# Kernel tuning notes

Measured on AMD Instinct MI355X. Metric: run time of the kernel, lower is better.

The kernel has to match this reference:

```python
import jax, jax.numpy as jnp
import numpy as np

NB, NWAY, NBASE, FEAT, SEM = 8, 16, 8000, 512, 300
TEMP = float(np.sqrt(FEAT))  # d_k = feat_dim // n_head = 512


def setup_inputs() -> dict:
    key = jax.random.key(0)
    ks = jax.random.split(key, 18)
    n = jax.random.normal
    s_q = float(np.sqrt(2.0 / (FEAT + FEAT)))   # std for w_qs/w_ks/w_vs (d_model + d_k)
    s_sem = float(np.sqrt(2.0 / 600.0))
    s_lin = float(np.sqrt(1.0 / 300.0))
    return {
        "support_feat": n(ks[0], (NB, NWAY, FEAT), jnp.float32),
        "base_weights": n(ks[1], (NB, NBASE, FEAT), jnp.float32),
        "support_seman": n(ks[2], (NB, NWAY, SEM), jnp.float32),
        "base_seman": n(ks[3], (NB, NBASE, SEM), jnp.float32),
        # map_sem: Linear(300,300) -> LeakyReLU(0.1) -> Linear(300,300); weights stored (in,out)
        "map_w1": n(ks[4], (SEM, SEM), jnp.float32) * s_lin,
        "map_b1": jnp.zeros((SEM,), jnp.float32),
        "map_w2": n(ks[5], (SEM, SEM), jnp.float32) * s_lin,
        "map_b2": jnp.zeros((SEM,), jnp.float32),
        # task fusion gates: Linear(feat+300 -> feat) and Linear(feat+300 -> 300)
        "visfuse_w": n(ks[6], (FEAT + SEM, FEAT), jnp.float32) * s_lin,
        "visfuse_b": jnp.zeros((FEAT,), jnp.float32),
        "semfuse_w": n(ks[7], (FEAT + SEM, SEM), jnp.float32) * s_lin,
        "semfuse_b": jnp.zeros((SEM,), jnp.float32),
        # MHA projections (bias-free), stored (in,out)
        "w_qs": n(ks[8], (FEAT, FEAT), jnp.float32) * s_q,
        "w_ks": n(ks[9], (FEAT, FEAT), jnp.float32) * s_q,
        "w_vs": n(ks[10], (FEAT, FEAT), jnp.float32) * s_q,
        "w_qs_sem": n(ks[11], (SEM, FEAT), jnp.float32) * s_sem,
        "w_ks_sem": n(ks[12], (SEM, FEAT), jnp.float32) * s_sem,
        "fc_w": n(ks[13], (FEAT, FEAT), jnp.float32) * s_q,
    }


def _map_sem(x, w1, b1, w2, b2):
    return jax.nn.leaky_relu(x @ w1 + b1, negative_slope=0.1) @ w2 + b2


def _forward(support_feat, base_weights, support_seman, base_seman,
             map_w1, map_b1, map_w2, map_b2,
             visfuse_w, visfuse_b, semfuse_w, semfuse_b,
             w_qs, w_ks, w_vs, w_qs_sem, w_ks_sem, fc_w):
    # semantic calibration of both support and base semantics (base_seman_calib=True)
    support_seman = _map_sem(support_seman, map_w1, b1=map_b1, w2=map_w2, b2=map_b2)  # (nb,nway,300)
    base_seman = _map_sem(base_seman, map_w1, b1=map_b1, w2=map_w2, b2=map_b2)        # (nb,N,300)

    # avg_task_mem over base classes (repeat over nway is a no-op for the mean)
    avg = jnp.concatenate([jnp.mean(base_weights, axis=1, keepdims=True),
                           jnp.mean(base_seman, axis=1, keepdims=True)], axis=-1)      # (nb,1,feat+300)
    gate_vis = jax.nn.sigmoid(avg @ visfuse_w + visfuse_b) + 1.0                       # (nb,1,feat)
    gate_sem = jax.nn.sigmoid(avg @ semfuse_w + semfuse_b) + 1.0                       # (nb,1,300)

    base_mem_vis = base_weights                 # un-gated value memory (v)
    k_vis = base_weights * gate_vis             # gated keys
    k_sem = base_seman * gate_sem               # gated semantic keys

    # projections (n_head=1, d_k=d_v=feat)
    q = support_feat @ w_qs                     # (nb,nway,feat)
    k = k_vis @ w_ks                            # (nb,N,feat)
    v = base_mem_vis @ w_vs                     # (nb,N,feat)
    q_tot = q + support_seman @ w_qs_sem        # semantic-fused q
    k_tot = k + k_sem @ w_ks_sem                # semantic-fused k

    # each support sample attends over the shared base memory of its episode
    attn_score = jnp.einsum('bwd,bnd->bwn', q_tot, k_tot) / TEMP                       # (nb,nway,N)
    attn = jax.nn.softmax(attn_score, axis=-1)
    out = jnp.einsum('bwn,bnd->bwd', attn, v) @ fc_w + support_feat                    # residual
    # SupportCalibrator returns (support_center, support_attn=attn_score)
    return out, attn_score


def reference(support_feat, base_weights, support_seman, base_seman,
              map_w1, map_b1, map_w2, map_b2,
              visfuse_w, visfuse_b, semfuse_w, semfuse_b,
              w_qs, w_ks, w_vs, w_qs_sem, w_ks_sem, fc_w):
    return _forward(support_feat, base_weights, support_seman, base_seman,
                    map_w1, map_b1, map_w2, map_b2,
                    visfuse_w, visfuse_b, semfuse_w, semfuse_b,
                    w_qs, w_ks, w_vs, w_qs_sem, w_ks_sem, fc_w)
```

## Files before the change

kernel.cpp:

```cpp
#include <hip/hip_runtime.h>

#define NB 8
#define NWAY 16
#define NBASE 8000
#define FEAT 512
#define SEM 300
#define CAT (FEAT + SEM)
#define HLD 304

typedef __attribute__((ext_vector_type(8))) short bf16x8;
typedef __attribute__((ext_vector_type(4))) float f32x4;
typedef __attribute__((ext_vector_type(8))) unsigned short us8;
typedef __attribute__((ext_vector_type(4))) unsigned short us4;
typedef __attribute__((ext_vector_type(2))) unsigned short us2;
typedef unsigned short us;

__device__ __forceinline__ us f2bf(float x) {
    union { float f; unsigned int u; } v; v.f = x;
    unsigned int r = v.u + 0x7FFFu + ((v.u >> 16) & 1u);
    return (us)(r >> 16);
}
__device__ __forceinline__ float bf2f(us u) {
    union { unsigned int u; float f; } v; v.u = ((unsigned int)u) << 16;
    return v.f;
}

constexpr long O_BWH   = 0L;
constexpr long O_H     = 65536000L;
constexpr long O_W1T   = 104448000L;
constexpr long O_W2T   = 104652800L;
constexpr long O_QWT   = 104857600L;
constexpr long O_WVST  = 106496000L;
constexpr long O_FCWT  = 107020288L;
constexpr long O_PQT   = 107544576L;
constexpr long O_PMAX  = 107759616L;
constexpr long O_PSUM  = 107791872L;
constexpr long O_RMAX  = 107824128L;
constexpr long O_RINV  = 107824640L;
constexpr long O_F     = 107825152L;
constexpr long O_MBW   = O_F;
constexpr long O_MH    = O_F + 16384;
constexpr long O_GV    = O_F + 25984;
constexpr long O_GS    = O_F + 42368;
constexpr long O_SSMH  = O_F + 77952;
constexpr long O_QTG   = O_F + 77952;
constexpr long O_OV    = O_F + 233600;
constexpr long O_SFH   = O_F + 540800;
constexpr long O_PSG   = O_F + 540800;
constexpr long O_H1G   = O_F + 671872;
constexpr long O_CC    = O_F + 802944;
constexpr long O_WKST  = O_F + 803456;
constexpr long O_WKSST = O_F + 1327744;
constexpr long O_W2N   = O_F + 1655424;
constexpr long O_SSCG  = O_F + 1860224;

__global__ void k_prep(const float* __restrict__ w1, const float* __restrict__ w2,
                       const float* __restrict__ wqs, const float* __restrict__ wqss,
                       const float* __restrict__ wvs, const float* __restrict__ fcw,
                       const float* __restrict__ wks, const float* __restrict__ wkss,
                       const float* __restrict__ sf, const float* __restrict__ ssm,
                       us* __restrict__ w1t, us* __restrict__ w2t, us* __restrict__ qwT,
                       us* __restrict__ wvsT, us* __restrict__ fcwT,
                       us* __restrict__ wksT, us* __restrict__ wkssT, us* __restrict__ w2n,
                       us* __restrict__ sfh, us* __restrict__ ssmh,
                       float* __restrict__ mz, float* __restrict__ cz, us* __restrict__ pqt) {
    long e = (long)blockIdx.x * 256 + threadIdx.x;
    switch (blockIdx.y) {
    case 0: if (e < 320 * 320) { int n = e / 320, k = e % 320;
            w1t[e] = f2bf((n < SEM && k < SEM) ? w1[(long)k * SEM + n] : 0.f); } break;
    case 1: if (e < 320 * 320) { int n = e / 320, k = e % 320;
            w2t[e] = f2bf((n < SEM && k < SEM) ? w2[(long)k * SEM + n] : 0.f); } break;
    case 2: if (e < 512 * 832) { int n = e / 832, k = e % 832;
            float v = 0.f;
            if (k < FEAT) v = wqs[(long)k * FEAT + n];
            else if (k < CAT) v = wqss[(long)(k - FEAT) * FEAT + n];
            qwT[e] = f2bf(v); } break;
    case 3: if (e < 512 * 512) { int n = e / 512, k = e % 512;
            wvsT[e] = f2bf(wvs[(long)k * FEAT + n]); } break;
    case 4: if (e < 512 * 512) { int n = e / 512, k = e % 512;
            fcwT[e] = f2bf(fcw[(long)k * FEAT + n]); } break;
    case 5:
        if (e < NB * FEAT + NB * SEM) mz[e] = 0.f;
        if (e < NB * NWAY) cz[e] = 0.f;
        if (e < 128 * 28) pqt[(e / 28) * 840 + 812 + (e % 28)] = 0;
        break;
    case 6: if (e < 512 * 512) wksT[e] = f2bf(wks[e]); break;
    case 7: if (e < 320 * 512) { int n = e / 512, k = e % 512;
            wkssT[e] = (n < SEM) ? f2bf(wkss[(long)n * FEAT + k]) : (us)0; } break;
    case 8: if (e < 320 * 320) { int n = e / 320, k = e % 320;
            w2n[e] = (n < SEM && k < SEM) ? f2bf(w2[(long)n * SEM + k]) : (us)0; } break;
    case 9: if (e < 128 * 512) sfh[e] = f2bf(sf[e]); break;
    case 10: if (e < 128 * 320) { int n = e / 320, k = e % 320;
            ssmh[e] = (k < SEM) ? f2bf(ssm[(long)n * SEM + k]) : (us)0; } break;
    }
}

__global__ __launch_bounds__(256) void k_cvt_mlp1(
        const float* __restrict__ bw, us* __restrict__ bwh, float* __restrict__ mbw,
        const us* __restrict__ ssmh, const us* __restrict__ w1t,
        const float* __restrict__ b1, us* __restrict__ h1g) {
    __shared__ float red[128][4];
    const int bid = blockIdx.x;
    const int t = threadIdx.x;
    if (bid < 10) {
        const int ctile = bid % 5, rh = bid / 5;
        const int wv = t >> 6, lane = t & 63;
        const int m16 = lane & 15, q = lane >> 4;
        const int nc0 = ctile * 64;
        const int n = nc0 + wv * 16 + m16;
        f32x4 acc[4];
        #pragma unroll
        for (int i = 0; i < 4; ++i) acc[i] = (f32x4){0.f, 0.f, 0.f, 0.f};
        for (int ks = 0; ks < 10; ++ks) {
            const int k = ks * 32 + q * 8;
            bf16x8 bb = *(const bf16x8*)(w1t + (long)n * 320 + k);
            #pragma unroll
            for (int mt = 0; mt < 4; ++mt) {
                bf16x8 a = *(const bf16x8*)(ssmh + (long)(rh * 64 + mt * 16 + m16) * 320 + k);
                acc[mt] = __builtin_amdgcn_mfma_f32_16x16x32_bf16(a, bb, acc[mt], 0, 0, 0);
            }
        }
        const int col = n;
        const float bias = (col < SEM) ? b1[col] : 0.f;
        #pragma unroll
        for (int mt = 0; mt < 4; ++mt)
            #pragma unroll
            for (int r = 0; r < 4; ++r) {
                float v = acc[mt][r] + bias;
                v = v > 0.f ? v : 0.1f * v;
                const int gr = rh * 64 + mt * 16 + q * 4 + r;
                h1g[(long)gr * 320 + col] = (col < SEM) ? f2bf(v) : (us)0;
            }
        return;
    }
    const int fb = bid - 10;
    const int b = fb / 125, ch = fb % 125;
    int cg = t & 127, rs = t >> 7;
    long base = ((long)b * NBASE + (long)ch * 64) * FEAT + cg * 4;
    float s0 = 0.f, s1 = 0.f, s2 = 0.f, s3 = 0.f;
    for (int r0 = rs * 4; r0 < 64; r0 += 8) {
        float4 v[4];
        #pragma unroll
        for (int u = 0; u < 4; ++u)
            v[u] = *(const float4*)(bw + base + (long)(r0 + u) * FEAT);
        #pragma unroll
        for (int u = 0; u < 4; ++u) {
            us4 o; o.x = f2bf(v[u].x); o.y = f2bf(v[u].y); o.z = f2bf(v[u].z); o.w = f2bf(v[u].w);
            *(us4*)(bwh + base + (long)(r0 + u) * FEAT) = o;
            s0 += v[u].x; s1 += v[u].y; s2 += v[u].z; s3 += v[u].w;
        }
    }
    if (rs == 1) { red[cg][0] = s0; red[cg][1] = s1; red[cg][2] = s2; red[cg][3] = s3; }
    __syncthreads();
    if (rs == 0) {
        atomicAdd(&mbw[b * FEAT + cg * 4 + 0], s0 + red[cg][0]);
        atomicAdd(&mbw[b * FEAT + cg * 4 + 1], s1 + red[cg][1]);
        atomicAdd(&mbw[b * FEAT + cg * 4 + 2], s2 + red[cg][2]);
        atomicAdd(&mbw[b * FEAT + cg * 4 + 3], s3 + red[cg][3]);
    }
}

__global__ __launch_bounds__(256, 2) void k_hg_mlp2(const float* __restrict__ X,
        const us* __restrict__ W1T, const float* __restrict__ b1,
        us* __restrict__ H, float* __restrict__ mh,
        const us* __restrict__ h1g, const us* __restrict__ w2t,
        const float* __restrict__ b2, us* __restrict__ sscg) {
    __shared__ char smem[128 * 304 * 2];
    const int bid = blockIdx.x;
    const int t = threadIdx.x;
    const int wv = t >> 6, lane = t & 63;
    const int m16 = lane & 15, q = lane >> 4;
    if (bid < 10) {
        const int ctile = bid % 5, rh = bid / 5;
        const int n = ctile * 64 + wv * 16 + m16;
        f32x4 acc[4];
        #pragma unroll
        for (int i = 0; i < 4; ++i) acc[i] = (f32x4){0.f, 0.f, 0.f, 0.f};
        for (int ks = 0; ks < 10; ++ks) {
            const int k = ks * 32 + q * 8;
            bf16x8 bb = *(const bf16x8*)(w2t + (long)n * 320 + k);
            #pragma unroll
            for (int mt = 0; mt < 4; ++mt) {
                bf16x8 a = *(const bf16x8*)(h1g + (long)(rh * 64 + mt * 16 + m16) * 320 + k);
                acc[mt] = __builtin_amdgcn_mfma_f32_16x16x32_bf16(a, bb, acc[mt], 0, 0, 0);
            }
        }
        const int col = n;
        const float bias = (col < SEM) ? b2[col] : 0.f;
        #pragma unroll
        for (int mt = 0; mt < 4; ++mt)
            #pragma unroll
            for (int r = 0; r < 4; ++r) {
                const int gr = rh * 64 + mt * 16 + q * 4 + r;
                sscg[(long)gr * 320 + col] = (col < SEM) ? f2bf(acc[mt][r] + bias) : (us)0;
            }
        return;
    }
    us (*As)[72] = (us(*)[72])smem;
    us (*Bs)[72] = (us(*)[72])(smem + 18432);
    us (*Cs)[HLD] = (us(*)[HLD])smem;
    const int fb = bid - 10;
    const int b = fb / 63;
    const int bm = (fb % 63) * 128;
    const long rowbase = (long)b * NBASE;
    f32x4 acc[8][5];
    #pragma unroll
    for (int i = 0; i < 8; ++i)
        #pragma unroll
        for (int j = 0; j < 5; ++j) acc[i][j] = (f32x4){0.f, 0.f, 0.f, 0.f};
    for (int ks = 0; ks < 5; ++ks) {
        const int k0 = ks * 64;
        #pragma unroll
        for (int it = 0; it < 8; ++it) {
            int c = t + it * 256;
            int row = c >> 4, j = c & 15;
            int gk = k0 + j * 4;
            float4 v = make_float4(0.f, 0.f, 0.f, 0.f);
            if (gk < SEM && bm + row < NBASE)
                v = *(const float4*)(X + (rowbase + bm + row) * SEM + gk);
            us4 u; u.x = f2bf(v.x); u.y = f2bf(v.y); u.z = f2bf(v.z); u.w = f2bf(v.w);
            *(us4*)(&As[row][j * 4]) = u;
        }
        #pragma unroll
        for (int it = 0; it < 10; ++it) {
            int c = t + it * 256;
            int n = c >> 3, j = c & 7;
            int4 v = *(const int4*)(W1T + (long)n * 320 + k0 + j * 8);
            *(int4*)(&Bs[n][j * 8]) = v;
        }
        __syncthreads();
        #pragma unroll
        for (int kc = 0; kc < 64; kc += 32) {
            bf16x8 a[8], bb[5];
            #pragma unroll
            for (int rt = 0; rt < 8; ++rt)
                a[rt] = *(const bf16x8*)(&As[rt * 16 + m16][kc + q * 8]);
            #pragma unroll
            for (int ct = 0; ct < 5; ++ct)
                bb[ct] = *(const bf16x8*)(&Bs[(wv * 5 + ct) * 16 + m16][kc + q * 8]);
            #pragma unroll
            for (int rt = 0; rt < 8; ++rt)
                #pragma unroll
                for (int ct = 0; ct < 5; ++ct)
                    acc[rt][ct] = __builtin_amdgcn_mfma_f32_16x16x32_bf16(a[rt], bb[ct], acc[rt][ct], 0, 0, 0);
        }
        __syncthreads();
    }
    float csum[5] = {0.f, 0.f, 0.f, 0.f, 0.f};
    #pragma unroll
    for (int ct = 0; ct < 5; ++ct) {
        int col = (wv * 5 + ct) * 16 + m16;
        float bias = (col < SEM) ? b1[col] : 0.f;
        #pragma unroll
        for (int rt = 0; rt < 8; ++rt) {
            int rl = rt * 16 + q * 4;
            #pragma unroll
            for (int r = 0; r < 4; ++r) {
                float v = acc[rt][ct][r] + bias;
                v = v > 0.f ? v : 0.1f * v;
                if (col < SEM && bm + rl + r < NBASE) {
                    Cs[rl + r][col] = f2bf(v);
                    csum[ct] += v;
                }
            }
        }
    }
    if (t < 128) *(us4*)(&Cs[t][300]) = (us4){0, 0, 0, 0};
    #pragma unroll
    for (int ct = 0; ct < 5; ++ct) {
        float s = csum[ct];
        s += __shfl_xor(s, 16);
        s += __shfl_xor(s, 32);
        int col = (wv * 5 + ct) * 16 + m16;
        if (q == 0 && col < SEM) atomicAdd(&mh[b * SEM + col], s);
    }
    __syncthreads();
    for (int i = t; i < 128 * 76; i += 256) {
        int row = i / 76, j = i % 76;
        if (bm + row < NBASE)
            *(us4*)(H + (rowbase + bm + row) * HLD + j * 4) = *(const us4*)(&Cs[row][j * 4]);
    }
}

__global__ __launch_bounds__(256) void k_gates_qtot(
        const float* __restrict__ mbw, const float* __restrict__ mh,
        const float* __restrict__ mw2, const float* __restrict__ mb2,
        const float* __restrict__ vfw, const float* __restrict__ vfb,
        const float* __restrict__ sfw, const float* __restrict__ sfb,
        float* __restrict__ gv, float* __restrict__ gs,
        const us* __restrict__ sfh, const us* __restrict__ sscg,
        const us* __restrict__ qwT, us* __restrict__ qtotg) {
    __shared__ float avgL[CAT];
    __shared__ float mhL[SEM];
    __shared__ float red[4][64];
    const int bid = blockIdx.x;
    const int t = threadIdx.x;
    if (bid < 16) {
        const int ctile = bid % 8, rh = bid / 8;
        const int wv = t >> 6, lane = t & 63;
        const int m16 = lane & 15, q = lane >> 4;
        const int n = ctile * 64 + wv * 16 + m16;
        f32x4 acc[4];
        #pragma unroll
        for (int i = 0; i < 4; ++i) acc[i] = (f32x4){0.f, 0.f, 0.f, 0.f};
        for (int ks = 0; ks < 26; ++ks) {
            const int k = ks * 32 + q * 8;
            bf16x8 bb = *(const bf16x8*)(qwT + (long)n * 832 + k);
            #pragma unroll
            for (int mt = 0; mt < 4; ++mt) {
                const int gr = rh * 64 + mt * 16 + m16;
                bf16x8 a = (k < FEAT)
                    ? *(const bf16x8*)(sfh + (long)gr * 512 + k)
                    : *(const bf16x8*)(sscg + (long)gr * 320 + (k - FEAT));
                acc[mt] = __builtin_amdgcn_mfma_f32_16x16x32_bf16(a, bb, acc[mt], 0, 0, 0);
            }
        }
        #pragma unroll
        for (int mt = 0; mt < 4; ++mt)
            #pragma unroll
            for (int r = 0; r < 4; ++r) {
                const int gr = rh * 64 + mt * 16 + q * 4 + r;
                qtotg[(long)gr * 512 + n] = f2bf(acc[mt][r]);
            }
        return;
    }
    const int tile = (bid - 16) % 13, b = (bid - 16) / 13;
    const float invN = 1.0f / NBASE;
    for (int i = t; i < SEM; i += 256) mhL[i] = mh[b * SEM + i] * invN;
    for (int i = t; i < FEAT; i += 256) avgL[i] = mbw[b * FEAT + i] * invN;
    __syncthreads();
    for (int s = t; s < SEM; s += 256) {
        float a = mb2[s];
        for (int c = 0; c < SEM; ++c) a += mhL[c] * mw2[(long)c * SEM + s];
        avgL[FEAT + s] = a;
    }
    __syncthreads();
    int l = t & 63, kq = t >> 6;
    float a = 0.f;
    if (tile < 8) {
        int f = tile * 64 + l;
        for (int c = kq * 203; c < kq * 203 + 203; ++c) a += avgL[c] * vfw[(long)c * FEAT + f];
        red[kq][l] = a;
        __syncthreads();
        if (kq == 0) {
            float s = red[0][l] + red[1][l] + red[2][l] + red[3][l] + vfb[f];
            gv[b * FEAT + f] = 1.f + 1.f / (1.f + expf(-s));
        }
    } else {
        int fs = (tile - 8) * 64 + l;
        if (fs < SEM)
            for (int c = kq * 203; c < kq * 203 + 203; ++c) a += avgL[c] * sfw[(long)c * SEM + fs];
        red[kq][l] = a;
        __syncthreads();
        if (kq == 0 && fs < SEM) {
            float s = red[0][l] + red[1][l] + red[2][l] + red[3][l] + sfb[fs];
            gs[b * SEM + fs] = 1.f + 1.f / (1.f + expf(-s));
        }
    }
}

__global__ __launch_bounds__(256) void k_projgate(
        const us* __restrict__ qtotg, const us* __restrict__ wksT,
        const us* __restrict__ wkssT, const float* __restrict__ gv,
        const float* __restrict__ gs, const float* __restrict__ b2,
        us* __restrict__ pqt, us* __restrict__ psemG, float* __restrict__ cconst) {
    const int bid = blockIdx.x;
    const int nslot = bid % 13, rh = bid / 13;
    const int t = threadIdx.x;
    const int wv = t >> 6, lane = t & 63;
    const int m16 = lane & 15, q = lane >> 4;
    const bool isv = (nslot < 8);
    const int nc0 = isv ? nslot * 64 : (nslot - 8) * 64;
    const us* BT = isv ? wksT : wkssT;
    const int n = nc0 + wv * 16 + m16;
    f32x4 acc[4];
    #pragma unroll
    for (int i = 0; i < 4; ++i) acc[i] = (f32x4){0.f, 0.f, 0.f, 0.f};
    for (int ks = 0; ks < 16; ++ks) {
        const int k = ks * 32 + q * 8;
        bf16x8 bb = *(const bf16x8*)(BT + (long)n * 512 + k);
        #pragma unroll
        for (int mt = 0; mt < 4; ++mt) {
            bf16x8 a = *(const bf16x8*)(qtotg + (long)(rh * 64 + mt * 16 + m16) * 512 + k);
            acc[mt] = __builtin_amdgcn_mfma_f32_16x16x32_bf16(a, bb, acc[mt], 0, 0, 0);
        }
    }
    const int col = n;
    if (isv) {
        #pragma unroll
        for (int mt = 0; mt < 4; ++mt)
            #pragma unroll
            for (int r = 0; r < 4; ++r) {
                const int gr = rh * 64 + mt * 16 + q * 4 + r;
                const int b = gr >> 4;
                pqt[(long)gr * 840 + col] = f2bf(acc[mt][r] * gv[b * FEAT + col]);
            }
    } else {
        const float b2c = (col < SEM) ? b2[col] : 0.f;
        #pragma unroll
        for (int mt = 0; mt < 4; ++mt)
            #pragma unroll
            for (int r = 0; r < 4; ++r) {
                const int gr = rh * 64 + mt * 16 + q * 4 + r;
                const int b = gr >> 4;
                float p = (col < SEM) ? acc[mt][r] * gs[b * SEM + col] : 0.f;
                psemG[(long)gr * 320 + col] = (col < SEM) ? f2bf(p) : (us)0;
                float ps = p * b2c;
                ps += __shfl_xor(ps, 1); ps += __shfl_xor(ps, 2);
                ps += __shfl_xor(ps, 4); ps += __shfl_xor(ps, 8);
                if (m16 == 0) atomicAdd(&cconst[b * NWAY + (gr & 15)], ps);
            }
    }
}

__global__ __launch_bounds__(256) void k_sem2(const us* __restrict__ psemG,
        const us* __restrict__ w2n, us* __restrict__ pqt) {
    const int bid = blockIdx.x;
    const int ctile = bid % 5, rh = bid / 5;
    const int t = threadIdx.x;
    const int wv = t >> 6, lane = t & 63;
    const int m16 = lane & 15, q = lane >> 4;
    const int n = ctile * 64 + wv * 16 + m16;
    f32x4 acc[4];
    #pragma unroll
    for (int i = 0; i < 4; ++i) acc[i] = (f32x4){0.f, 0.f, 0.f, 0.f};
    for (int ks = 0; ks < 10; ++ks) {
        const int k = ks * 32 + q * 8;
        bf16x8 bb = *(const bf16x8*)(w2n + (long)n * 320 + k);
        #pragma unroll
        for (int mt = 0; mt < 4; ++mt) {
            bf16x8 a = *(const bf16x8*)(psemG + (long)(rh * 64 + mt * 16 + m16) * 320 + k);
            acc[mt] = __builtin_amdgcn_mfma_f32_16x16x32_bf16(a, bb, acc[mt], 0, 0, 0);
        }
    }
    const int col = n;
    if (col < SEM) {
        #pragma unroll
        for (int mt = 0; mt < 4; ++mt)
            #pragma unroll
            for (int r = 0; r < 4; ++r) {
                const int gr = rh * 64 + mt * 16 + q * 4 + r;
                pqt[(long)gr * 840 + 512 + col] = f2bf(acc[mt][r]);
            }
    }
}

__global__ __launch_bounds__(256) void k_scores_mfma(const us* __restrict__ bwh,
        const us* __restrict__ h, const us* __restrict__ pqt,
        const float* __restrict__ cconst, float* __restrict__ scores,
        float* __restrict__ pmax, float* __restrict__ psum) {
    __shared__ us As[128][72];
    __shared__ us Bs[NWAY][840];
    __shared__ float sred[4][16];
    const int b = blockIdx.y;
    const int bm = blockIdx.x * 128;
    const int t = threadIdx.x;
    const int wv = t >> 6, lane = t & 63;
    const int m16 = lane & 15, q = lane >> 4;
    for (int c = t; c < NWAY * 105; c += 256) {
        int n = c / 105, j = c % 105;
        *(int4*)(&Bs[n][j * 8]) = *(const int4*)(pqt + ((long)b * NWAY + n) * 840 + j * 8);
    }
    f32x4 acc[2];
    acc[0] = (f32x4){0, 0, 0, 0};
    acc[1] = (f32x4){0, 0, 0, 0};
    for (int ks = 0; ks < 13; ++ks) {
        int k0 = ks * 64;
        #pragma unroll
        for (int it = 0; it < 4; ++it) {
            int c = t + it * 256;
            int row = c >> 3, j = c & 7;
            int gm = bm + row, gk = k0 + j * 8;
            us8 u = (us8){0, 0, 0, 0, 0, 0, 0, 0};
            if (gk < FEAT)      u = *(const us8*)(bwh + ((long)b * NBASE + gm) * FEAT + gk);
            else if (gk < CAT)  u = *(const us8*)(h + ((long)b * NBASE + gm) * HLD + (gk - FEAT));
            *(us8*)(&As[row][j * 8]) = u;
        }
        __syncthreads();
        #pragma unroll
        for (int kc = 0; kc < 64; kc += 32) {
            bf16x8 bb = *(const bf16x8*)(&Bs[m16][k0 + kc + q * 8]);
            #pragma unroll
            for (int rt = 0; rt < 2; ++rt) {
                bf16x8 a = *(const bf16x8*)(&As[wv * 32 + rt * 16 + m16][kc + q * 8]);
                acc[rt] = __builtin_amdgcn_mfma_f32_16x16x32_bf16(a, bb, acc[rt], 0, 0, 0);
            }
        }
        __syncthreads();
    }
    const float invT = 0.04419417382415922f;
    float cadd = cconst[b * NWAY + m16];
    float vals[8];
    #pragma unroll
    for (int rt = 0; rt < 2; ++rt) {
        int nrow = bm + wv * 32 + rt * 16 + q * 4;
        #pragma unroll
        for (int r = 0; r < 4; ++r) {
            float v = (nrow + r < NBASE) ? (acc[rt][r] + cadd) * invT : -1e30f;
            vals[rt * 4 + r] = v;
        }
        if (nrow + 3 < NBASE) {
            float4 st = make_float4(vals[rt * 4], vals[rt * 4 + 1], vals[rt * 4 + 2], vals[rt * 4 + 3]);
            *(float4*)(scores + ((long)b * NWAY + m16) * NBASE + nrow) = st;
        } else {
            for (int r = 0; r < 4; ++r)
                if (nrow + r < NBASE)
                    scores[((long)b * NWAY + m16) * NBASE + nrow + r] = vals[rt * 4 + r];
        }
    }
    float lm = vals[0];
    #pragma unroll
    for (int i = 1; i < 8; ++i) lm = fmaxf(lm, vals[i]);
    lm = fmaxf(lm, __shfl_xor(lm, 16));
    lm = fmaxf(lm, __shfl_xor(lm, 32));
    if (q == 0) sred[wv][m16] = lm;
    __syncthreads();
    float bmax = fmaxf(fmaxf(sred[0][m16], sred[1][m16]), fmaxf(sred[2][m16], sred[3][m16]));
    __syncthreads();
    float ls = 0.f;
    #pragma unroll
    for (int i = 0; i < 8; ++i) ls += __expf(vals[i] - bmax);
    ls += __shfl_xor(ls, 16);
    ls += __shfl_xor(ls, 32);
    if (q == 0) sred[wv][m16] = ls;
    __syncthreads();
    if (wv == 0 && lane < 16) {
        float tot = sred[0][m16] + sred[1][m16] + sred[2][m16] + sred[3][m16];
        pmax[((long)b * NWAY + m16) * 63 + blockIdx.x] = bmax;
        psum[((long)b * NWAY + m16) * 63 + blockIdx.x] = tot;
    }
}

__global__ void k_combine(const float* __restrict__ pmax, const float* __restrict__ psum,
                          float* __restrict__ rmax, float* __restrict__ rinv,
                          float* __restrict__ ov) {
    int b = blockIdx.x, t = threadIdx.x;
    float4 z = make_float4(0.f, 0.f, 0.f, 0.f);
    for (int i = t; i < 2048; i += 256)
        *(float4*)(ov + ((long)b * 2048 + i) * 4) = z;
    int w = t >> 4, l = t & 15;
    long base = ((long)b * NWAY + w) * 63;
    float m = -1e30f;
    for (int i = l; i < 63; i += 16) m = fmaxf(m, pmax[base + i]);
    m = fmaxf(m, __shfl_xor(m, 1)); m = fmaxf(m, __shfl_xor(m, 2));
    m = fmaxf(m, __shfl_xor(m, 4)); m = fmaxf(m, __shfl_xor(m, 8));
    float s = 0.f;
    for (int i = l; i < 63; i += 16) s += psum[base + i] * __expf(pmax[base + i] - m);
    s += __shfl_xor(s, 1); s += __shfl_xor(s, 2);
    s += __shfl_xor(s, 4); s += __shfl_xor(s, 8);
    if (l == 0) { rmax[b * NWAY + w] = m; rinv[b * NWAY + w] = 1.0f / s; }
}

__global__ void k_ov(const float* __restrict__ scores, const float* __restrict__ rmax,
                     const float* __restrict__ rinv, const us* __restrict__ bwh,
                     float* __restrict__ ov) {
    int b = blockIdx.x, ch = blockIdx.y;
    int t = threadIdx.x;
    __shared__ float pr[NWAY][160];
    for (int i = t; i < NWAY * 160; i += 256) {
        int w = i / 160, j = i % 160;
        float sc = scores[((long)b * NWAY + w) * NBASE + (long)ch * 160 + j];
        pr[w][j] = __expf(sc - rmax[b * NWAY + w]) * rinv[b * NWAY + w];
    }
    __syncthreads();
    float a0[NWAY], a1[NWAY];
    #pragma unroll
    for (int w = 0; w < NWAY; ++w) { a0[w] = 0.f; a1[w] = 0.f; }
    const us* bp = bwh + ((long)b * NBASE + (long)ch * 160) * FEAT + 2 * t;
    for (int j0 = 0; j0 < 160; j0 += 8) {
        us2 u[8];
        #pragma unroll
        for (int uu = 0; uu < 8; ++uu)
            u[uu] = *(const us2*)(bp + (long)(j0 + uu) * FEAT);
        #pragma unroll
        for (int uu = 0; uu < 8; ++uu) {
            float v0 = bf2f(u[uu].x), v1 = bf2f(u[uu].y);
            #pragma unroll
            for (int w = 0; w < NWAY; ++w) {
                a0[w] += pr[w][j0 + uu] * v0;
                a1[w] += pr[w][j0 + uu] * v1;
            }
        }
    }
    for (int w = 0; w < NWAY; ++w) {
        atomicAdd(&ov[((long)b * NWAY + w) * FEAT + 2 * t], a0[w]);
        atomicAdd(&ov[((long)b * NWAY + w) * FEAT + 2 * t + 1], a1[w]);
    }
}

__global__ __launch_bounds__(256) void k_out1(const float* __restrict__ ov,
        const us* __restrict__ wvsT, us* __restrict__ tmp) {
    const int bid = blockIdx.x;
    const int ctile = bid & 7, rh = bid >> 3;
    const int t = threadIdx.x;
    const int wv = t >> 6, lane = t & 63;
    const int m16 = lane & 15, q = lane >> 4;
    const int n = ctile * 64 + wv * 16 + m16;
    f32x4 acc[4];
    #pragma unroll
    for (int i = 0; i < 4; ++i) acc[i] = (f32x4){0.f, 0.f, 0.f, 0.f};
    #pragma unroll 4
    for (int ks = 0; ks < 16; ++ks) {
        const int k = ks * 32 + q * 8;
        bf16x8 bb = *(const bf16x8*)(wvsT + (long)n * 512 + k);
        #pragma unroll
        for (int mt = 0; mt < 4; ++mt) {
            const float* ap = ov + (long)(rh * 64 + mt * 16 + m16) * 512 + k;
            float4 x = *(const float4*)ap, y = *(const float4*)(ap + 4);
            bf16x8 a;
            a[0] = (short)f2bf(x.x); a[1] = (short)f2bf(x.y);
            a[2] = (short)f2bf(x.z); a[3] = (short)f2bf(x.w);
            a[4] = (short)f2bf(y.x); a[5] = (short)f2bf(y.y);
            a[6] = (short)f2bf(y.z); a[7] = (short)f2bf(y.w);
            acc[mt] = __builtin_amdgcn_mfma_f32_16x16x32_bf16(a, bb, acc[mt], 0, 0, 0);
        }
    }
    #pragma unroll
    for (int mt = 0; mt < 4; ++mt)
        #pragma unroll
        for (int r = 0; r < 4; ++r) {
            const int gr = rh * 64 + mt * 16 + q * 4 + r;
            tmp[(long)gr * 512 + n] = f2bf(acc[mt][r]);
        }
}

__global__ __launch_bounds__(256) void k_out2(const us* __restrict__ tmp,
        const us* __restrict__ fcwT, const float* __restrict__ sf,
        float* __restrict__ out) {
    const int bid = blockIdx.x;
    const int ctile = bid & 7, rh = bid >> 3;
    const int t = threadIdx.x;
    const int wv = t >> 6, lane = t & 63;
    const int m16 = lane & 15, q = lane >> 4;
    const int n = ctile * 64 + wv * 16 + m16;
    f32x4 acc[4];
    #pragma unroll
    for (int i = 0; i < 4; ++i) acc[i] = (f32x4){0.f, 0.f, 0.f, 0.f};
    #pragma unroll 4
    for (int ks = 0; ks < 16; ++ks) {
        const int k = ks * 32 + q * 8;
        bf16x8 bb = *(const bf16x8*)(fcwT + (long)n * 512 + k);
        #pragma unroll
        for (int mt = 0; mt < 4; ++mt) {
            bf16x8 a = *(const bf16x8*)(tmp + (long)(rh * 64 + mt * 16 + m16) * 512 + k);
            acc[mt] = __builtin_amdgcn_mfma_f32_16x16x32_bf16(a, bb, acc[mt], 0, 0, 0);
        }
    }
    #pragma unroll
    for (int mt = 0; mt < 4; ++mt)
        #pragma unroll
        for (int r = 0; r < 4; ++r) {
            const long gr = rh * 64 + mt * 16 + q * 4 + r;
            out[gr * FEAT + n] = acc[mt][r] + sf[gr * FEAT + n];
        }
}

extern "C" void kernel_launch(void* const* d_in, const int* in_sizes, int n_in,
                              void* d_out, int out_size, void* d_ws, size_t ws_size,
                              hipStream_t stream) {
    (void)in_sizes; (void)n_in; (void)out_size; (void)ws_size;
    const float* sf   = (const float*)d_in[0];
    const float* bw   = (const float*)d_in[1];
    const float* ssm  = (const float*)d_in[2];
    const float* bsm  = (const float*)d_in[3];
    const float* mw1  = (const float*)d_in[4];
    const float* mb1  = (const float*)d_in[5];
    const float* mw2  = (const float*)d_in[6];
    const float* mb2  = (const float*)d_in[7];
    const float* vfw  = (const float*)d_in[8];
    const float* vfb  = (const float*)d_in[9];
    const float* sfw  = (const float*)d_in[10];
    const float* sfb  = (const float*)d_in[11];
    const float* wqs  = (const float*)d_in[12];
    const float* wks  = (const float*)d_in[13];
    const float* wvs  = (const float*)d_in[14];
    const float* wqss = (const float*)d_in[15];
    const float* wkss = (const float*)d_in[16];
    const float* fcw  = (const float*)d_in[17];

    float* out = (float*)d_out;
    float* scores = out + NB * NWAY * FEAT;

    char* wsb = (char*)d_ws;
    us* bwh    = (us*)(wsb + O_BWH);
    us* h      = (us*)(wsb + O_H);
    us* w1t    = (us*)(wsb + O_W1T);
    us* w2t    = (us*)(wsb + O_W2T);
    us* qwT    = (us*)(wsb + O_QWT);
    us* wvsT   = (us*)(wsb + O_WVST);
    us* fcwT   = (us*)(wsb + O_FCWT);
    us* pqt    = (us*)(wsb + O_PQT);
    us* wksT   = (us*)(wsb + O_WKST);
    us* wkssT  = (us*)(wsb + O_WKSST);
    us* w2n    = (us*)(wsb + O_W2N);
    us* sfh    = (us*)(wsb + O_SFH);
    us* ssmh   = (us*)(wsb + O_SSMH);
    us* h1g    = (us*)(wsb + O_H1G);
    us* sscg   = (us*)(wsb + O_SSCG);
    us* qtotg  = (us*)(wsb + O_QTG);
    us* psemG  = (us*)(wsb + O_PSG);
    float* pmax   = (float*)(wsb + O_PMAX);
    float* psum   = (float*)(wsb + O_PSUM);
    float* rmax   = (float*)(wsb + O_RMAX);
    float* rinv   = (float*)(wsb + O_RINV);
    float* mbw    = (float*)(wsb + O_MBW);
    float* mh     = (float*)(wsb + O_MH);
    float* gv     = (float*)(wsb + O_GV);
    float* gs     = (float*)(wsb + O_GS);
    float* ov     = (float*)(wsb + O_OV);
    float* cconst = (float*)(wsb + O_CC);

    k_prep<<<dim3(1664, 11), 256, 0, stream>>>(mw1, mw2, wqs, wqss, wvs, fcw, wks, wkss,
                                               sf, ssm,
                                               w1t, w2t, qwT, wvsT, fcwT, wksT, wkssT, w2n,
                                               sfh, ssmh, mbw, cconst, pqt);
    k_cvt_mlp1<<<1010, 256, 0, stream>>>(bw, bwh, mbw, ssmh, w1t, mb1, h1g);
    k_hg_mlp2<<<514, 256, 0, stream>>>(bsm, w1t, mb1, h, mh, h1g, w2t, mb2, sscg);
    k_gates_qtot<<<120, 256, 0, stream>>>(mbw, mh, mw2, mb2, vfw, vfb, sfw, sfb, gv, gs,
                                          sfh, sscg, qwT, qtotg);
    k_projgate<<<26, 256, 0, stream>>>(qtotg, wksT, wkssT, gv, gs, mb2, pqt, psemG, cconst);
    k_sem2<<<10, 256, 0, stream>>>(psemG, w2n, pqt);
    k_scores_mfma<<<dim3(63, NB), 256, 0, stream>>>(bwh, h, pqt, cconst, scores, pmax, psum);
    k_combine<<<NB, 256, 0, stream>>>(pmax, psum, rmax, rinv, ov);
    k_ov<<<dim3(NB, 50), 256, 0, stream>>>(scores, rmax, rinv, bwh, ov);
    k_out1<<<16, 256, 0, stream>>>(ov, wvsT, qtotg);
    k_out2<<<16, 256, 0, stream>>>(qtotg, fcwT, sf, out);
}
```

Baseline: 522.2 us.

## Tile weight transposes via shared memory, fold combine into k_ov, halve GEMM row tiles

```diff
diff --git a/kernel.cpp b/kernel.cpp
--- a/kernel.cpp
+++ b/kernel.cpp
@@ -54,43 +54,76 @@
 constexpr long O_W2N   = O_F + 1655424;
 constexpr long O_SSCG  = O_F + 1860224;
 
-__global__ void k_prep(const float* __restrict__ w1, const float* __restrict__ w2,
-                       const float* __restrict__ wqs, const float* __restrict__ wqss,
-                       const float* __restrict__ wvs, const float* __restrict__ fcw,
-                       const float* __restrict__ wks, const float* __restrict__ wkss,
-                       const float* __restrict__ sf, const float* __restrict__ ssm,
-                       us* __restrict__ w1t, us* __restrict__ w2t, us* __restrict__ qwT,
-                       us* __restrict__ wvsT, us* __restrict__ fcwT,
+__global__ __launch_bounds__(256) void k_tr(
+        const float* __restrict__ w1, const float* __restrict__ w2,
+        const float* __restrict__ wqs, const float* __restrict__ wqss,
+        const float* __restrict__ wvs, const float* __restrict__ fcw,
+        us* __restrict__ w1t, us* __restrict__ w2t, us* __restrict__ qwT,
+        us* __restrict__ wvsT, us* __restrict__ fcwT) {
+    __shared__ us tile[64][66];
+    const int cs = blockIdx.y;
+    const int t = threadIdx.x;
+    int tilesK, N, K, LD, srcN, srcK;
+    const float* S0;
+    us* D;
+    switch (cs) {
+    case 0:  tilesK = 5;  N = 320; K = 320; LD = 320; S0 = w1;  D = w1t;  srcN = 300; srcK = 300; break;
+    case 1:  tilesK = 5;  N = 320; K = 320; LD = 320; S0 = w2;  D = w2t;  srcN = 300; srcK = 300; break;
+    case 2:  tilesK = 13; N = 512; K = 832; LD = 832; S0 = wqs; D = qwT;  srcN = 512; srcK = 812; break;
+    case 3:  tilesK = 8;  N = 512; K = 512; LD = 512; S0 = wvs; D = wvsT; srcN = 512; srcK = 512; break;
+    default: tilesK = 8;  N = 512; K = 512; LD = 512; S0 = fcw; D = fcwT; srcN = 512; srcK = 512; break;
+    }
+    const int ntiles = tilesK * (N >> 6);
+    if ((int)blockIdx.x >= ntiles) return;
+    const int tk = (blockIdx.x % tilesK) * 64;
+    const int tn = (blockIdx.x / tilesK) * 64;
+    #pragma unroll
+    for (int i = 0; i < 16; ++i) {
+        int idx = t + i * 256;
+        int kk = idx >> 6, nn = idx & 63;
+        int k = tk + kk, n = tn + nn;
+        float v = 0.f;
+        if (n < srcN && k < srcK) {
+            if (cs == 2) v = (k < FEAT) ? wqs[(long)k * 512 + n] : wqss[(long)(k - FEAT) * 512 + n];
+            else v = S0[(long)k * srcN + n];
+        }
+        tile[kk][nn] = f2bf(v);
+    }
+    __syncthreads();
+    #pragma unroll
+    for (int i = 0; i < 8; ++i) {
+        int idx = t + i * 256;
+        int nn = idx >> 5, kp = (idx & 31) * 2;
+        int n = tn + nn, k = tk + kp;
+        if (n < N && k < K) {
+            us2 o; o.x = tile[kp][nn]; o.y = tile[kp + 1][nn];
+            *(us2*)(D + (long)n * LD + k) = o;
+        }
+    }
+}
+
+__global__ void k_prep(const float* __restrict__ wks, const float* __restrict__ wkss,
+                       const float* __restrict__ w2, const float* __restrict__ sf,
+                       const float* __restrict__ ssm,
                        us* __restrict__ wksT, us* __restrict__ wkssT, us* __restrict__ w2n,
                        us* __restrict__ sfh, us* __restrict__ ssmh,
-                       float* __restrict__ mz, float* __restrict__ cz, us* __restrict__ pqt) {
+                       float* __restrict__ mz, float* __restrict__ cz,
+                       us* __restrict__ pqt, float* __restrict__ ovz) {
     long e = (long)blockIdx.x * 256 + threadIdx.x;
     switch (blockIdx.y) {
-    case 0: if (e < 320 * 320) { int n = e / 320, k = e % 320;
-            w1t[e] = f2bf((n < SEM && k < SEM) ? w1[(long)k * SEM + n] : 0.f); } break;
-    case 1: if (e < 320 * 320) { int n = e / 320, k = e % 320;
-            w2t[e] = f2bf((n < SEM && k < SEM) ? w2[(long)k * SEM + n] : 0.f); } break;
-    case 2: if (e < 512 * 832) { int n = e / 832, k = e % 832;
-            float v = 0.f;
-            if (k < FEAT) v = wqs[(long)k * FEAT + n];
-            else if (k < CAT) v = wqss[(long)(k - FEAT) * FEAT + n];
-            qwT[e] = f2bf(v); } break;
-    case 3: if (e < 512 * 512) { int n = e / 512, k = e % 512;
-            wvsT[e] = f2bf(wvs[(long)k * FEAT + n]); } break;
-    case 4: if (e < 512 * 512) { int n = e / 512, k = e % 512;
-            fcwT[e] = f2bf(fcw[(long)k * FEAT + n]); } break;
-    case 5:
+    case 0:
         if (e < NB * FEAT + NB * SEM) mz[e] = 0.f;
         if (e < NB * NWAY) cz[e] = 0.f;
         if (e < 128 * 28) pqt[(e / 28) * 840 + 812 + (e % 28)] = 0;
+        if (e < NB * NWAY * FEAT) ovz[e] = 0.f;
         break;
-    case 6: if (e < 512 * 512) wksT[e] = f2bf(wks[e]); break;
-    case 7: if (e < 320 * 512) { int n = e / 512, k = e % 512;
+    case 1: if (e < 512 * 512) wksT[e] = f2bf(wks[e]); break;
+    case 2: if (e < 320 * 512) { int n = e / 512, k = e % 512;
             wkssT[e] = (n < SEM) ? f2bf(wkss[(long)n * FEAT + k]) : (us)0; } break;
-    case 8: if (e < 320 * 320) { int n = e / 320, k = e % 320;
+    case 3: if (e < 320 * 320) { int n = e / 320, k = e % 320;
             w2n[e] = (n < SEM && k < SEM) ? f2bf(w2[(long)n * SEM + k]) : (us)0; } break;
-    case 9: if (e < 128 * 512) sfh[e] = f2bf(sf[e]); break;
-    case 10: if (e < 128 * 320) { int n = e / 320, k = e % 320;
+    case 4: if (e < 128 * 512) sfh[e] = f2bf(sf[e]); break;
+    case 5: if (e < 128 * 320) { int n = e / 320, k = e % 320;
             ssmh[e] = (k < SEM) ? f2bf(ssm[(long)n * SEM + k]) : (us)0; } break;
     }
 }
@@ -106,8 +139,7 @@
         const int ctile = bid % 5, rh = bid / 5;
         const int wv = t >> 6, lane = t & 63;
         const int m16 = lane & 15, q = lane >> 4;
-        const int nc0 = ctile * 64;
-        const int n = nc0 + wv * 16 + m16;
+        const int n = ctile * 64 + wv * 16 + m16;
         f32x4 acc[4];
         #pragma unroll
         for (int i = 0; i < 4; ++i) acc[i] = (f32x4){0.f, 0.f, 0.f, 0.f};
@@ -295,20 +327,20 @@
     __shared__ float red[4][64];
     const int bid = blockIdx.x;
     const int t = threadIdx.x;
-    if (bid < 16) {
+    if (bid < 32) {
         const int ctile = bid % 8, rh = bid / 8;
         const int wv = t >> 6, lane = t & 63;
         const int m16 = lane & 15, q = lane >> 4;
         const int n = ctile * 64 + wv * 16 + m16;
-        f32x4 acc[4];
-        #pragma unroll
-        for (int i = 0; i < 4; ++i) acc[i] = (f32x4){0.f, 0.f, 0.f, 0.f};
+        f32x4 acc[2];
+        acc[0] = (f32x4){0.f, 0.f, 0.f, 0.f};
+        acc[1] = (f32x4){0.f, 0.f, 0.f, 0.f};
         for (int ks = 0; ks < 26; ++ks) {
             const int k = ks * 32 + q * 8;
             bf16x8 bb = *(const bf16x8*)(qwT + (long)n * 832 + k);
             #pragma unroll
-            for (int mt = 0; mt < 4; ++mt) {
-                const int gr = rh * 64 + mt * 16 + m16;
+            for (int mt = 0; mt < 2; ++mt) {
+                const int gr = rh * 32 + mt * 16 + m16;
                 bf16x8 a = (k < FEAT)
                     ? *(const bf16x8*)(sfh + (long)gr * 512 + k)
                     : *(const bf16x8*)(sscg + (long)gr * 320 + (k - FEAT));
@@ -316,15 +348,15 @@
             }
         }
         #pragma unroll
-        for (int mt = 0; mt < 4; ++mt)
+        for (int mt = 0; mt < 2; ++mt)
             #pragma unroll
             for (int r = 0; r < 4; ++r) {
-                const int gr = rh * 64 + mt * 16 + q * 4 + r;
+                const int gr = rh * 32 + mt * 16 + q * 4 + r;
                 qtotg[(long)gr * 512 + n] = f2bf(acc[mt][r]);
             }
         return;
     }
-    const int tile = (bid - 16) % 13, b = (bid - 16) / 13;
+    const int tile = (bid - 32) % 13, b = (bid - 32) / 13;
     const float invN = 1.0f / NBASE;
     for (int i = t; i < SEM; i += 256) mhL[i] = mh[b * SEM + i] * invN;
     for (int i = t; i < FEAT; i += 256) avgL[i] = mbw[b * FEAT + i] * invN;
@@ -373,35 +405,35 @@
     const int nc0 = isv ? nslot * 64 : (nslot - 8) * 64;
     const us* BT = isv ? wksT : wkssT;
     const int n = nc0 + wv * 16 + m16;
-    f32x4 acc[4];
-    #pragma unroll
-    for (int i = 0; i < 4; ++i) acc[i] = (f32x4){0.f, 0.f, 0.f, 0.f};
+    f32x4 acc[2];
+    acc[0] = (f32x4){0.f, 0.f, 0.f, 0.f};
+    acc[1] = (f32x4){0.f, 0.f, 0.f, 0.f};
     for (int ks = 0; ks < 16; ++ks) {
         const int k = ks * 32 + q * 8;
         bf16x8 bb = *(const bf16x8*)(BT + (long)n * 512 + k);
         #pragma unroll
-        for (int mt = 0; mt < 4; ++mt) {
-            bf16x8 a = *(const bf16x8*)(qtotg + (long)(rh * 64 + mt * 16 + m16) * 512 + k);
+        for (int mt = 0; mt < 2; ++mt) {
+            bf16x8 a = *(const bf16x8*)(qtotg + (long)(rh * 32 + mt * 16 + m16) * 512 + k);
             acc[mt] = __builtin_amdgcn_mfma_f32_16x16x32_bf16(a, bb, acc[mt], 0, 0, 0);
         }
     }
     const int col = n;
     if (isv) {
         #pragma unroll
-        for (int mt = 0; mt < 4; ++mt)
+        for (int mt = 0; mt < 2; ++mt)
             #pragma unroll
             for (int r = 0; r < 4; ++r) {
-                const int gr = rh * 64 + mt * 16 + q * 4 + r;
+                const int gr = rh * 32 + mt * 16 + q * 4 + r;
                 const int b = gr >> 4;
                 pqt[(long)gr * 840 + col] = f2bf(acc[mt][r] * gv[b * FEAT + col]);
             }
     } else {
         const float b2c = (col < SEM) ? b2[col] : 0.f;
         #pragma unroll
-        for (int mt = 0; mt < 4; ++mt)
+        for (int mt = 0; mt < 2; ++mt)
             #pragma unroll
             for (int r = 0; r < 4; ++r) {
-                const int gr = rh * 64 + mt * 16 + q * 4 + r;
+                const int gr = rh * 32 + mt * 16 + q * 4 + r;
                 const int b = gr >> 4;
                 float p = (col < SEM) ? acc[mt][r] * gs[b * SEM + col] : 0.f;
                 psemG[(long)gr * 320 + col] = (col < SEM) ? f2bf(p) : (us)0;
@@ -421,25 +453,25 @@
     const int wv = t >> 6, lane = t & 63;
     const int m16 = lane & 15, q = lane >> 4;
     const int n = ctile * 64 + wv * 16 + m16;
-    f32x4 acc[4];
-    #pragma unroll
-    for (int i = 0; i < 4; ++i) acc[i] = (f32x4){0.f, 0.f, 0.f, 0.f};
+    f32x4 acc[2];
+    acc[0] = (f32x4){0.f, 0.f, 0.f, 0.f};
+    acc[1] = (f32x4){0.f, 0.f, 0.f, 0.f};
     for (int ks = 0; ks < 10; ++ks) {
         const int k = ks * 32 + q * 8;
         bf16x8 bb = *(const bf16x8*)(w2n + (long)n * 320 + k);
         #pragma unroll
-        for (int mt = 0; mt < 4; ++mt) {
-            bf16x8 a = *(const bf16x8*)(psemG + (long)(rh * 64 + mt * 16 + m16) * 320 + k);
+        for (int mt = 0; mt < 2; ++mt) {
+            bf16x8 a = *(const bf16x8*)(psemG + (long)(rh * 32 + mt * 16 + m16) * 320 + k);
             acc[mt] = __builtin_amdgcn_mfma_f32_16x16x32_bf16(a, bb, acc[mt], 0, 0, 0);
         }
     }
     const int col = n;
     if (col < SEM) {
         #pragma unroll
-        for (int mt = 0; mt < 4; ++mt)
+        for (int mt = 0; mt < 2; ++mt)
             #pragma unroll
             for (int r = 0; r < 4; ++r) {
-                const int gr = rh * 64 + mt * 16 + q * 4 + r;
+                const int gr = rh * 32 + mt * 16 + q * 4 + r;
                 pqt[(long)gr * 840 + 512 + col] = f2bf(acc[mt][r]);
             }
     }
@@ -531,36 +563,31 @@
     }
 }
 
-__global__ void k_combine(const float* __restrict__ pmax, const float* __restrict__ psum,
-                          float* __restrict__ rmax, float* __restrict__ rinv,
-                          float* __restrict__ ov) {
-    int b = blockIdx.x, t = threadIdx.x;
-    float4 z = make_float4(0.f, 0.f, 0.f, 0.f);
-    for (int i = t; i < 2048; i += 256)
-        *(float4*)(ov + ((long)b * 2048 + i) * 4) = z;
-    int w = t >> 4, l = t & 15;
-    long base = ((long)b * NWAY + w) * 63;
-    float m = -1e30f;
-    for (int i = l; i < 63; i += 16) m = fmaxf(m, pmax[base + i]);
-    m = fmaxf(m, __shfl_xor(m, 1)); m = fmaxf(m, __shfl_xor(m, 2));
-    m = fmaxf(m, __shfl_xor(m, 4)); m = fmaxf(m, __shfl_xor(m, 8));
-    float s = 0.f;
-    for (int i = l; i < 63; i += 16) s += psum[base + i] * __expf(pmax[base + i] - m);
-    s += __shfl_xor(s, 1); s += __shfl_xor(s, 2);
-    s += __shfl_xor(s, 4); s += __shfl_xor(s, 8);
-    if (l == 0) { rmax[b * NWAY + w] = m; rinv[b * NWAY + w] = 1.0f / s; }
-}
-
-__global__ void k_ov(const float* __restrict__ scores, const float* __restrict__ rmax,
-                     const float* __restrict__ rinv, const us* __restrict__ bwh,
+__global__ void k_ov(const float* __restrict__ scores, const float* __restrict__ pmax,
+                     const float* __restrict__ psum, const us* __restrict__ bwh,
                      float* __restrict__ ov) {
     int b = blockIdx.x, ch = blockIdx.y;
     int t = threadIdx.x;
     __shared__ float pr[NWAY][160];
+    __shared__ float rm[NWAY], ri[NWAY];
+    {
+        int w = t >> 4, l = t & 15;
+        long base = ((long)b * NWAY + w) * 63;
+        float m = -1e30f;
+        for (int i = l; i < 63; i += 16) m = fmaxf(m, pmax[base + i]);
+        m = fmaxf(m, __shfl_xor(m, 1)); m = fmaxf(m, __shfl_xor(m, 2));
+        m = fmaxf(m, __shfl_xor(m, 4)); m = fmaxf(m, __shfl_xor(m, 8));
+        float s = 0.f;
+        for (int i = l; i < 63; i += 16) s += psum[base + i] * __expf(pmax[base + i] - m);
+        s += __shfl_xor(s, 1); s += __shfl_xor(s, 2);
+        s += __shfl_xor(s, 4); s += __shfl_xor(s, 8);
+        if (l == 0) { rm[w] = m; ri[w] = 1.0f / s; }
+    }
+    __syncthreads();
     for (int i = t; i < NWAY * 160; i += 256) {
         int w = i / 160, j = i % 160;
         float sc = scores[((long)b * NWAY + w) * NBASE + (long)ch * 160 + j];
-        pr[w][j] = __expf(sc - rmax[b * NWAY + w]) * rinv[b * NWAY + w];
+        pr[w][j] = __expf(sc - rm[w]) * ri[w];
     }
     __syncthreads();
     float a0[NWAY], a1[NWAY];
@@ -596,16 +623,16 @@
     const int wv = t >> 6, lane = t & 63;
     const int m16 = lane & 15, q = lane >> 4;
     const int n = ctile * 64 + wv * 16 + m16;
-    f32x4 acc[4];
-    #pragma unroll
-    for (int i = 0; i < 4; ++i) acc[i] = (f32x4){0.f, 0.f, 0.f, 0.f};
+    f32x4 acc[2];
+    acc[0] = (f32x4){0.f, 0.f, 0.f, 0.f};
+    acc[1] = (f32x4){0.f, 0.f, 0.f, 0.f};
     #pragma unroll 4
     for (int ks = 0; ks < 16; ++ks) {
         const int k = ks * 32 + q * 8;
         bf16x8 bb = *(const bf16x8*)(wvsT + (long)n * 512 + k);
         #pragma unroll
-        for (int mt = 0; mt < 4; ++mt) {
-            const float* ap = ov + (long)(rh * 64 + mt * 16 + m16) * 512 + k;
+        for (int mt = 0; mt < 2; ++mt) {
+            const float* ap = ov + (long)(rh * 32 + mt * 16 + m16) * 512 + k;
             float4 x = *(const float4*)ap, y = *(const float4*)(ap + 4);
             bf16x8 a;
             a[0] = (short)f2bf(x.x); a[1] = (short)f2bf(x.y);
@@ -616,10 +643,10 @@
         }
     }
     #pragma unroll
-    for (int mt = 0; mt < 4; ++mt)
+    for (int mt = 0; mt < 2; ++mt)
         #pragma unroll
         for (int r = 0; r < 4; ++r) {
-            const int gr = rh * 64 + mt * 16 + q * 4 + r;
+            const int gr = rh * 32 + mt * 16 + q * 4 + r;
             tmp[(long)gr * 512 + n] = f2bf(acc[mt][r]);
         }
 }
@@ -633,24 +660,24 @@
     const int wv = t >> 6, lane = t & 63;
     const int m16 = lane & 15, q = lane >> 4;
     const int n = ctile * 64 + wv * 16 + m16;
-    f32x4 acc[4];
-    #pragma unroll
-    for (int i = 0; i < 4; ++i) acc[i] = (f32x4){0.f, 0.f, 0.f, 0.f};
+    f32x4 acc[2];
+    acc[0] = (f32x4){0.f, 0.f, 0.f, 0.f};
+    acc[1] = (f32x4){0.f, 0.f, 0.f, 0.f};
     #pragma unroll 4
     for (int ks = 0; ks < 16; ++ks) {
         const int k = ks * 32 + q * 8;
         bf16x8 bb = *(const bf16x8*)(fcwT + (long)n * 512 + k);
         #pragma unroll
-        for (int mt = 0; mt < 4; ++mt) {
-            bf16x8 a = *(const bf16x8*)(tmp + (long)(rh * 64 + mt * 16 + m16) * 512 + k);
+        for (int mt = 0; mt < 2; ++mt) {
+            bf16x8 a = *(const bf16x8*)(tmp + (long)(rh * 32 + mt * 16 + m16) * 512 + k);
             acc[mt] = __builtin_amdgcn_mfma_f32_16x16x32_bf16(a, bb, acc[mt], 0, 0, 0);
         }
     }
     #pragma unroll
-    for (int mt = 0; mt < 4; ++mt)
+    for (int mt = 0; mt < 2; ++mt)
         #pragma unroll
         for (int r = 0; r < 4; ++r) {
-            const long gr = rh * 64 + mt * 16 + q * 4 + r;
+            const long gr = rh * 32 + mt * 16 + q * 4 + r;
             out[gr * FEAT + n] = acc[mt][r] + sf[gr * FEAT + n];
         }
 }
@@ -701,8 +728,6 @@
     us* psemG  = (us*)(wsb + O_PSG);
     float* pmax   = (float*)(wsb + O_PMAX);
     float* psum   = (float*)(wsb + O_PSUM);
-    float* rmax   = (float*)(wsb + O_RMAX);
-    float* rinv   = (float*)(wsb + O_RINV);
     float* mbw    = (float*)(wsb + O_MBW);
     float* mh     = (float*)(wsb + O_MH);
     float* gv     = (float*)(wsb + O_GV);
@@ -710,19 +735,19 @@
     float* ov     = (float*)(wsb + O_OV);
     float* cconst = (float*)(wsb + O_CC);
 
-    k_prep<<<dim3(1664, 11), 256, 0, stream>>>(mw1, mw2, wqs, wqss, wvs, fcw, wks, wkss,
-                                               sf, ssm,
-                                               w1t, w2t, qwT, wvsT, fcwT, wksT, wkssT, w2n,
-                                               sfh, ssmh, mbw, cconst, pqt);
+    k_tr<<<dim3(104, 5), 256, 0, stream>>>(mw1, mw2, wqs, wqss, wvs, fcw,
+                                           w1t, w2t, qwT, wvsT, fcwT);
+    k_prep<<<dim3(1024, 6), 256, 0, stream>>>(wks, wkss, mw2, sf, ssm,
+                                              wksT, wkssT, w2n, sfh, ssmh,
+                                              mbw, cconst, pqt, ov);
     k_cvt_mlp1<<<1010, 256, 0, stream>>>(bw, bwh, mbw, ssmh, w1t, mb1, h1g);
     k_hg_mlp2<<<514, 256, 0, stream>>>(bsm, w1t, mb1, h, mh, h1g, w2t, mb2, sscg);
-    k_gates_qtot<<<120, 256, 0, stream>>>(mbw, mh, mw2, mb2, vfw, vfb, sfw, sfb, gv, gs,
+    k_gates_qtot<<<136, 256, 0, stream>>>(mbw, mh, mw2, mb2, vfw, vfb, sfw, sfb, gv, gs,
                                           sfh, sscg, qwT, qtotg);
-    k_projgate<<<26, 256, 0, stream>>>(qtotg, wksT, wkssT, gv, gs, mb2, pqt, psemG, cconst);
-    k_sem2<<<10, 256, 0, stream>>>(psemG, w2n, pqt);
+    k_projgate<<<52, 256, 0, stream>>>(qtotg, wksT, wkssT, gv, gs, mb2, pqt, psemG, cconst);
+    k_sem2<<<20, 256, 0, stream>>>(psemG, w2n, pqt);
     k_scores_mfma<<<dim3(63, NB), 256, 0, stream>>>(bwh, h, pqt, cconst, scores, pmax, psum);
-    k_combine<<<NB, 256, 0, stream>>>(pmax, psum, rmax, rinv, ov);
-    k_ov<<<dim3(NB, 50), 256, 0, stream>>>(scores, rmax, rinv, bwh, ov);
-    k_out1<<<16, 256, 0, stream>>>(ov, wvsT, qtotg);
-    k_out2<<<16, 256, 0, stream>>>(qtotg, fcwT, sf, out);
-}
+    k_ov<<<dim3(NB, 50), 256, 0, stream>>>(scores, pmax, psum, bwh, ov);
+    k_out1<<<32, 256, 0, stream>>>(ov, wvsT, qtotg);
+    k_out2<<<32, 256, 0, stream>>>(qtotg, fcwT, sf, out);
+}
```

Result: faster. 496.2 us (-5.0%).
